# Performance work log

Hardware: AMD Instinct MI355X
Metric: run time of the kernel (lower is better)

## Reference

```python
import jax, jax.numpy as jnp
import numpy as np

N = 100000        # nodes
E = 3200000       # edges (avg degree 32)
B = 64            # graphs in the batch
IN_DIM = 128
HEADS = 4
C1 = 8            # conv1 out_channels per head
C2 = 4            # conv2 out_channels per head
OUT_DIM = 10
EPS = 1e-16       # PyG softmax denominator eps


def _lin(key, fan_in, fan_out):
    return jax.random.normal(key, (fan_in, fan_out), jnp.float32) / np.sqrt(fan_in)


def setup_inputs() -> dict:
    key = jax.random.key(0)
    ks = jax.random.split(key, 16)
    x = jax.random.normal(ks[0], (N, IN_DIM), jnp.float32)
    edge_index = jax.random.randint(ks[1], (2, E), 0, N)
    batch = jnp.sort(jax.random.randint(ks[2], (N,), 0, B))
    d1 = HEADS * C1  # 32
    d2 = HEADS * C2  # 16
    inp = {
        "x": x, "edge_index": edge_index, "batch": batch,
        # conv1 (TransformerConv in=128 -> heads*8 = 32)
        "Wq1": _lin(ks[3], IN_DIM, d1), "bq1": jnp.zeros((d1,), jnp.float32),
        "Wk1": _lin(ks[4], IN_DIM, d1), "bk1": jnp.zeros((d1,), jnp.float32),
        "Wv1": _lin(ks[5], IN_DIM, d1), "bv1": jnp.zeros((d1,), jnp.float32),
        "Ws1": _lin(ks[6], IN_DIM, d1), "bs1": jnp.zeros((d1,), jnp.float32),
        # conv2 (in=32 -> heads*4 = 16)
        "Wq2": _lin(ks[7], d1, d2), "bq2": jnp.zeros((d2,), jnp.float32),
        "Wk2": _lin(ks[8], d1, d2), "bk2": jnp.zeros((d2,), jnp.float32),
        "Wv2": _lin(ks[9], d1, d2), "bv2": jnp.zeros((d2,), jnp.float32),
        "Ws2": _lin(ks[10], d1, d2), "bs2": jnp.zeros((d2,), jnp.float32),
        # fc (16 -> 10)
        "Wfc": _lin(ks[11], d2, OUT_DIM), "bfc": jnp.zeros((OUT_DIM,), jnp.float32),
    }
    return inp


def transformer_conv(x, src, dst, Wq, bq, Wk, bk, Wv, bv, Ws, bs, heads):
    n = x.shape[0]
    hc = Wq.shape[1]
    c = hc // heads
    q = (x @ Wq + bq).reshape(n, heads, c)
    k = (x @ Wk + bk).reshape(n, heads, c)
    v = (x @ Wv + bv).reshape(n, heads, c)
    # edge-wise attention logits: query at dst, key at src -> [E, H]
    alpha = jnp.einsum('ehc,ehc->eh', q[dst], k[src]) / np.sqrt(c).astype(np.float32)
    # segment softmax over incoming edges of each dst node
    amax = jax.ops.segment_max(alpha, dst, num_segments=n)           # [N,H]
    ea = jnp.exp(alpha - amax[dst])
    denom = jax.ops.segment_sum(ea, dst, num_segments=n)             # [N,H]
    w = ea / (denom[dst] + EPS)                                      # [E,H]
    msg = v[src] * w[:, :, None]                                     # [E,H,C]
    out = jax.ops.segment_sum(msg, dst, num_segments=n).reshape(n, hc)
    return out + x @ Ws + bs  # root/skip connection


def reference(x, edge_index, batch,
              Wq1, bq1, Wk1, bk1, Wv1, bv1, Ws1, bs1,
              Wq2, bq2, Wk2, bk2, Wv2, bv2, Ws2, bs2,
              Wfc, bfc):
    src, dst = edge_index[0], edge_index[1]
    h = transformer_conv(x, src, dst, Wq1, bq1, Wk1, bk1, Wv1, bv1, Ws1, bs1, HEADS)
    h = jax.nn.relu(h)
    h = transformer_conv(h, src, dst, Wq2, bq2, Wk2, bk2, Wv2, bv2, Ws2, bs2, HEADS)
    h = jax.nn.relu(h)
    # global mean pool per graph
    sums = jax.ops.segment_sum(h, batch, num_segments=B)             # [B,16]
    cnt = jax.ops.segment_sum(jnp.ones((h.shape[0],), h.dtype), batch, num_segments=B)
    pooled = sums / jnp.maximum(cnt, 1.0)[:, None]
    return pooled @ Wfc + bfc                                        # [B,OUT_DIM]
```

## Files before the change

kernel.cpp:

```cpp
#include <hip/hip_runtime.h>

#define HEADS 4
#define EPS 1e-16f
#define NR 256
#define EPB 2048
#define XPAD 132

typedef float floatx2 __attribute__((ext_vector_type(2)));

__device__ inline int rangeOf(int dst, int rdiv, float rinv) {
    int q = (int)((float)dst * rinv);
    if (q > NR - 1) q = NR - 1;
    if ((long long)q * rdiv > dst) --q;
    else if ((long long)(q + 1) * rdiv <= dst) ++q;
    return q;
}

__global__ __launch_bounds__(256) void scatter_count(
    const int* __restrict__ ei, int E, int rdiv, float rinv,
    int* __restrict__ pcnt)
{
    __shared__ int cnt[NR];
    int b = blockIdx.x, t = threadIdx.x;
    int b0 = b * EPB;
    int nloc = min(EPB, E - b0);
    cnt[t] = 0;
    __syncthreads();
    #pragma unroll
    for (int u = 0; u < 8; ++u) {
        int li = u * 256 + t;
        if (li < nloc)
            atomicAdd(&cnt[rangeOf(ei[E + b0 + li], rdiv, rinv)], 1);
    }
    __syncthreads();
    pcnt[(size_t)b * NR + t] = cnt[t];
}

__global__ __launch_bounds__(256) void qprefix(
    int* __restrict__ pcnt, int nb, int* __restrict__ qtot)
{
    __shared__ int part[256];
    int q = blockIdx.x, t = threadIdx.x;
    int per = (nb + 255) >> 8;
    int lo = t * per, hi = min(lo + per, nb);
    int s = 0;
    for (int b = lo; b < hi; ++b) s += pcnt[(size_t)b * NR + q];
    part[t] = s;
    __syncthreads();
    for (int off = 1; off < 256; off <<= 1) {
        int a = (t >= off) ? part[t - off] : 0;
        __syncthreads();
        part[t] += a;
        __syncthreads();
    }
    if (t == 255) qtot[q] = part[255];
    int pre = (t == 0) ? 0 : part[t - 1];
    for (int b = lo; b < hi; ++b) {
        int c = pcnt[(size_t)b * NR + q];
        pcnt[(size_t)b * NR + q] = pre;
        pre += c;
    }
}

__global__ void qscan(const int* __restrict__ qtot, int* __restrict__ rstart)
{
    __shared__ int tmp[NR];
    int t = threadIdx.x;
    tmp[t] = qtot[t];
    __syncthreads();
    for (int off = 1; off < NR; off <<= 1) {
        int a = (t >= off) ? tmp[t - off] : 0;
        __syncthreads();
        tmp[t] += a;
        __syncthreads();
    }
    rstart[t] = (t == 0) ? 0 : tmp[t - 1];
    if (t == NR - 1) rstart[NR] = tmp[NR - 1];
}

__global__ __launch_bounds__(256) void scatter_place(
    const int* __restrict__ ei, int E, int rdiv, float rinv,
    const int* __restrict__ pcnt, const int* __restrict__ rstart,
    int* __restrict__ rsrc, int* __restrict__ rdst)
{
    __shared__ int2 lrec[EPB];
    __shared__ unsigned char lq[EPB];
    __shared__ int cnt[NR], base[NR], scn[NR];
    int b = blockIdx.x, t = threadIdx.x;
    int b0 = b * EPB;
    int nloc = min(EPB, E - b0);
    cnt[t] = 0;
    __syncthreads();
    int myq[8], myoff[8];
    int2 myrec[8];
    #pragma unroll
    for (int u = 0; u < 8; ++u) {
        int li = u * 256 + t;
        if (li < nloc) {
            int e = b0 + li;
            int sv = ei[e], dv = ei[E + e];
            int q = rangeOf(dv, rdiv, rinv);
            myq[u] = q;
            myrec[u] = make_int2(sv, dv);
            myoff[u] = atomicAdd(&cnt[q], 1);
        } else myq[u] = -1;
    }
    __syncthreads();
    scn[t] = cnt[t];
    __syncthreads();
    for (int off = 1; off < 256; off <<= 1) {
        int a = (t >= off) ? scn[t - off] : 0;
        __syncthreads();
        scn[t] += a;
        __syncthreads();
    }
    base[t] = (t == 0) ? 0 : scn[t - 1];
    __syncthreads();
    #pragma unroll
    for (int u = 0; u < 8; ++u) {
        if (myq[u] >= 0) {
            int slot = base[myq[u]] + myoff[u];
            lrec[slot] = myrec[u];
            lq[slot] = (unsigned char)myq[u];
        }
    }
    __syncthreads();
    #pragma unroll
    for (int u = 0; u < 8; ++u) {
        int s2 = u * 256 + t;
        if (s2 < nloc) {
            int q = lq[s2];
            int g = rstart[q] + pcnt[(size_t)b * NR + q] + (s2 - base[q]);
            int2 r = lrec[s2];
            rsrc[g] = r.x;
            rdst[g] = r.y;
        }
    }
}

__global__ __launch_bounds__(256) void deg_range(
    const int* __restrict__ rdst, const int* __restrict__ rstart,
    int* __restrict__ deg, int* __restrict__ row_ptr,
    int* __restrict__ phd, int n, int rdiv, int E)
{
    __shared__ int h[512];
    __shared__ int psum[256];
    __shared__ int hd[256];
    int q = blockIdx.x, t = threadIdx.x;
    int lo = q * rdiv, hi = min(lo + rdiv, n);
    int nn = hi - lo;
    if (nn <= 0) {
        phd[q * 256 + t] = 0;
        if (t == 0 && q == NR - 1) row_ptr[n] = E;
        return;
    }
    h[t] = 0; h[t + 256] = 0; hd[t] = 0;
    __syncthreads();
    int rlo = rstart[q], rhi = rstart[q + 1];
    for (int i = rlo + t; i < rhi; i += 256)
        atomicAdd(&h[rdst[i] - lo], 1);
    __syncthreads();
    int s0 = h[2 * t], s1 = h[2 * t + 1];
    psum[t] = s0 + s1;
    __syncthreads();
    for (int off = 1; off < 256; off <<= 1) {
        int a = (t >= off) ? psum[t - off] : 0;
        __syncthreads();
        psum[t] += a;
        __syncthreads();
    }
    int base = rlo + ((t == 0) ? 0 : psum[t - 1]);
    if (2 * t < nn) {
        row_ptr[lo + 2 * t] = base;
        deg[lo + 2 * t] = s0;
        atomicAdd(&hd[min(s0, 255)], 1);
    }
    if (2 * t + 1 < nn) {
        row_ptr[lo + 2 * t + 1] = base + s0;
        deg[lo + 2 * t + 1] = s1;
        atomicAdd(&hd[min(s1, 255)], 1);
    }
    if (t == 0 && q == NR - 1) row_ptr[n] = E;
    __syncthreads();
    phd[q * 256 + t] = hd[t];
}

__global__ __launch_bounds__(256) void dsort_scanA(
    int* __restrict__ phd, int* __restrict__ tot)
{
    __shared__ int tmp[256];
    int bin = blockIdx.x, t = threadIdx.x;
    int v = phd[t * 256 + bin];
    tmp[t] = v;
    __syncthreads();
    for (int off = 1; off < 256; off <<= 1) {
        int a = (t >= off) ? tmp[t - off] : 0;
        __syncthreads();
        tmp[t] += a;
        __syncthreads();
    }
    phd[t * 256 + bin] = tmp[t] - v;
    if (t == 255) tot[bin] = tmp[255];
}

__global__ void dsort_scanB(int* __restrict__ tot)
{
    __shared__ int tmp[256];
    int t = threadIdx.x;
    int v = tot[t];
    tmp[t] = v;
    __syncthreads();
    for (int off = 1; off < 256; off <<= 1) {
        int a = (t >= off) ? tmp[t - off] : 0;
        __syncthreads();
        tmp[t] += a;
        __syncthreads();
    }
    tot[t] = tmp[t] - v;
}

__global__ __launch_bounds__(256) void dsort_addC(
    int* __restrict__ phd, const int* __restrict__ tot)
{
    int t = threadIdx.x;
    phd[blockIdx.x * 256 + t] += tot[t];
}

__global__ __launch_bounds__(256) void place_range(
    const int* __restrict__ rsrc, const int* __restrict__ rdst,
    const int* __restrict__ rstart, const int* __restrict__ row_ptr,
    const int* __restrict__ deg, const int* __restrict__ phd,
    int* __restrict__ col, int* __restrict__ order, int n, int rdiv)
{
    __shared__ int cur[512];
    __shared__ int lcur[256];
    int q = blockIdx.x, t = threadIdx.x;
    int lo = q * rdiv, hi = min(lo + rdiv, n);
    int nn = hi - lo;
    if (nn <= 0) return;
    for (int i = t; i < nn; i += 256) cur[i] = row_ptr[lo + i];
    lcur[t] = phd[q * 256 + t];
    __syncthreads();
    int rlo = rstart[q], rhi = rstart[q + 1];
    for (int i = rlo + t; i < rhi; i += 256) {
        int pos = atomicAdd(&cur[rdst[i] - lo], 1);
        col[pos] = rsrc[i];
    }
    for (int i = t; i < nn; i += 256) {
        int pos = atomicAdd(&lcur[min(deg[lo + i], 255)], 1);
        order[pos] = lo + i;
    }
}

__global__ __launch_bounds__(256) void proj1_kernel(
    const float* __restrict__ x,
    const float* __restrict__ Wq, const float* __restrict__ bq,
    const float* __restrict__ Wk, const float* __restrict__ bk,
    const float* __restrict__ Wv, const float* __restrict__ bv,
    const float* __restrict__ Ws, const float* __restrict__ bs,
    float* __restrict__ qs1, unsigned char* __restrict__ kv1, int n)
{
    __shared__ float Wl[128][64];
    __shared__ float xl[64][XPAD];
    int half = blockIdx.x & 1;
    for (int i = threadIdx.x; i < 128 * 64; i += 256) {
        int k = i >> 6, c = i & 63;
        int gc = half * 64 + c;
        int sub = gc >> 5, j = gc & 31;
        const float* W = (sub == 0) ? Wq : (sub == 1) ? Wk : (sub == 2) ? Wv : Ws;
        Wl[k][c] = W[k * 32 + j];
    }
    int col4 = (threadIdx.x & 15) * 4;
    int gcol4 = half * 64 + col4;
    int sub = gcol4 >> 5, j = gcol4 & 31;
    float4 bias4;
    {
        const float* b = (sub == 0) ? bq : (sub == 1) ? bk : (sub == 2) ? bv : bs;
        bias4 = *(const float4*)(b + j);
    }
    int rb = (threadIdx.x >> 4) * 4;
    __syncthreads();
    int rstride = (gridDim.x >> 1) * 64;
    for (int row0 = (blockIdx.x >> 1) * 64; row0 < n; row0 += rstride) {
        #pragma unroll
        for (int u = 0; u < 8; ++u) {
            int i = threadIdx.x + u * 256;
            int r = i >> 5, c4 = (i & 31) * 4;
            int gr = row0 + r;
            float4 xv = (gr < n) ? *(const float4*)(x + (size_t)gr * 128 + c4)
                                 : make_float4(0.f, 0.f, 0.f, 0.f);
            *(float4*)(&xl[r][c4]) = xv;
        }
        __syncthreads();
        float4 a0 = bias4, a1 = bias4, a2 = bias4, a3 = bias4;
        #pragma unroll 2
        for (int k = 0; k < 128; k += 4) {
            float4 xv0 = *(const float4*)(&xl[rb + 0][k]);
            float4 xv1 = *(const float4*)(&xl[rb + 1][k]);
            float4 xv2 = *(const float4*)(&xl[rb + 2][k]);
            float4 xv3 = *(const float4*)(&xl[rb + 3][k]);
            float4 w0 = *(const float4*)(&Wl[k + 0][col4]);
            float4 w1 = *(const float4*)(&Wl[k + 1][col4]);
            float4 w2 = *(const float4*)(&Wl[k + 2][col4]);
            float4 w3 = *(const float4*)(&Wl[k + 3][col4]);
            a0.x += xv0.x*w0.x + xv0.y*w1.x + xv0.z*w2.x + xv0.w*w3.x;
            a0.y += xv0.x*w0.y + xv0.y*w1.y + xv0.z*w2.y + xv0.w*w3.y;
            a0.z += xv0.x*w0.z + xv0.y*w1.z + xv0.z*w2.z + xv0.w*w3.z;
            a0.w += xv0.x*w0.w + xv0.y*w1.w + xv0.z*w2.w + xv0.w*w3.w;
            a1.x += xv1.x*w0.x + xv1.y*w1.x + xv1.z*w2.x + xv1.w*w3.x;
            a1.y += xv1.x*w0.y + xv1.y*w1.y + xv1.z*w2.y + xv1.w*w3.y;
            a1.z += xv1.x*w0.z + xv1.y*w1.z + xv1.z*w2.z + xv1.w*w3.z;
            a1.w += xv1.x*w0.w + xv1.y*w1.w + xv1.z*w2.w + xv1.w*w3.w;
            a2.x += xv2.x*w0.x + xv2.y*w1.x + xv2.z*w2.x + xv2.w*w3.x;
            a2.y += xv2.x*w0.y + xv2.y*w1.y + xv2.z*w2.y + xv2.w*w3.y;
            a2.z += xv2.x*w0.z + xv2.y*w1.z + xv2.z*w2.z + xv2.w*w3.z;
            a2.w += xv2.x*w0.w + xv2.y*w1.w + xv2.z*w2.w + xv2.w*w3.w;
            a3.x += xv3.x*w0.x + xv3.y*w1.x + xv3.z*w2.x + xv3.w*w3.x;
            a3.y += xv3.x*w0.y + xv3.y*w1.y + xv3.z*w2.y + xv3.w*w3.y;
            a3.z += xv3.x*w0.z + xv3.y*w1.z + xv3.z*w2.z + xv3.w*w3.z;
            a3.w += xv3.x*w0.w + xv3.y*w1.w + xv3.z*w2.w + xv3.w*w3.w;
        }
        #pragma unroll
        for (int r = 0; r < 4; ++r) {
            int row = row0 + rb + r;
            if (row < n) {
                float4 acc = (r == 0) ? a0 : (r == 1) ? a1 : (r == 2) ? a2 : a3;
                if (sub == 0)
                    *(float4*)(qs1 + (size_t)row * 64 + j) = acc;
                else if (sub == 3)
                    *(float4*)(qs1 + (size_t)row * 64 + 32 + j) = acc;
                else {
                    unsigned u8 = __builtin_amdgcn_cvt_pk_fp8_f32(acc.x, acc.y, 0u, false);
                    u8 = __builtin_amdgcn_cvt_pk_fp8_f32(acc.z, acc.w, u8, true);
                    *(unsigned*)(kv1 + (size_t)row * 64 + ((sub == 1) ? 0 : 32) + j) = u8;
                }
            }
        }
        __syncthreads();
    }
}

__global__ __launch_bounds__(256) void proj2_kernel(
    const float* __restrict__ h1,
    const float* __restrict__ Wq, const float* __restrict__ bq,
    const float* __restrict__ Wk, const float* __restrict__ bk,
    const float* __restrict__ Wv, const float* __restrict__ bv,
    const float* __restrict__ Ws, const float* __restrict__ bs,
    float* __restrict__ qs2, unsigned char* __restrict__ kv2, int n)
{
    __shared__ float Wl[32][64];
    __shared__ float bl[64];
    __shared__ float xl[4][32];
    for (int i = threadIdx.x; i < 32 * 64; i += 256) {
        int k = i >> 6, c = i & 63;
        int sub = c >> 4, j = c & 15;
        const float* W = (sub == 0) ? Wq : (sub == 1) ? Wk : (sub == 2) ? Wv : Ws;
        Wl[k][c] = W[k * 16 + j];
    }
    if (threadIdx.x < 64) {
        int c = threadIdx.x, sub = c >> 4, j = c & 15;
        const float* b = (sub == 0) ? bq : (sub == 1) ? bk : (sub == 2) ? bv : bs;
        bl[c] = b[j];
    }
    __syncthreads();
    int r = threadIdx.x >> 6, col = threadIdx.x & 63;
    int sub = col >> 4, j = col & 15;
    for (int row0 = blockIdx.x * 4; row0 < n; row0 += gridDim.x * 4) {
        int li = threadIdx.x;
        if (li < 128) {
            int rr = row0 + (li >> 5);
            if (rr < n) xl[li >> 5][li & 31] = h1[(size_t)rr * 32 + (li & 31)];
        }
        __syncthreads();
        int row = row0 + r;
        if (row < n) {
            float acc = bl[col];
            #pragma unroll
            for (int k = 0; k < 32; ++k) acc += xl[r][k] * Wl[k][col];
            if (sub == 0)       qs2[(size_t)row * 32 + j] = acc;
            else if (sub == 3)  qs2[(size_t)row * 32 + 16 + j] = acc;
            else {
                unsigned u8 = __builtin_amdgcn_cvt_pk_fp8_f32(acc, 0.f, 0u, false);
                kv2[(size_t)row * 32 + ((sub == 1) ? 0 : 16) + j] = (unsigned char)(u8 & 0xFF);
            }
        }
        __syncthreads();
    }
}

__global__ __launch_bounds__(256) void gather_conv1(
    const int* __restrict__ row_ptr, const int* __restrict__ order,
    const int* __restrict__ col, const float* __restrict__ qs1,
    const unsigned char* __restrict__ kv1, float* __restrict__ h1, int n)
{
    int tid = blockIdx.x * 256 + threadIdx.x;
    if (tid >= n * HEADS) return;
    int node = order[tid >> 2], h = tid & 3;
    const float4* qp = (const float4*)(qs1 + (size_t)node * 64 + h * 8);
    float4 q0 = qp[0], q1 = qp[1];
    int start = row_ptr[node], d = row_ptr[node + 1] - start;
    float m = -INFINITY, s = 0.f;
    float a0x=0,a0y=0,a0z=0,a0w=0,a1x=0,a1y=0,a1z=0,a1w=0;
    uint2 ku = make_uint2(0,0), vu = make_uint2(0,0);
    if (d > 0) {
        const unsigned char* b0 = kv1 + (size_t)col[start] * 64;
        ku = *(const uint2*)(b0 + h * 8);
        vu = *(const uint2*)(b0 + 32 + h * 8);
    }
    for (int i = 0; i < d; ++i) {
        uint2 kn = ku, vn = vu;
        if (i + 1 < d) {
            const unsigned char* nb = kv1 + (size_t)col[start + i + 1] * 64;
            kn = *(const uint2*)(nb + h * 8);
            vn = *(const uint2*)(nb + 32 + h * 8);
        }
        floatx2 k01 = __builtin_amdgcn_cvt_pk_f32_fp8(ku.x, false);
        floatx2 k23 = __builtin_amdgcn_cvt_pk_f32_fp8(ku.x, true);
        floatx2 k45 = __builtin_amdgcn_cvt_pk_f32_fp8(ku.y, false);
        floatx2 k67 = __builtin_amdgcn_cvt_pk_f32_fp8(ku.y, true);
        float a = (q0.x*k01.x + q0.y*k01.y + q0.z*k23.x + q0.w*k23.y
                 + q1.x*k45.x + q1.y*k45.y + q1.z*k67.x + q1.w*k67.y)
                * 0.35355339059327373f;
        float mn = fmaxf(m, a);
        float corr = __expf(m - mn);
        float ea = __expf(a - mn);
        s = s * corr + ea;
        floatx2 v01 = __builtin_amdgcn_cvt_pk_f32_fp8(vu.x, false);
        floatx2 v23 = __builtin_amdgcn_cvt_pk_f32_fp8(vu.x, true);
        floatx2 v45 = __builtin_amdgcn_cvt_pk_f32_fp8(vu.y, false);
        floatx2 v67 = __builtin_amdgcn_cvt_pk_f32_fp8(vu.y, true);
        a0x = a0x*corr + ea*v01.x; a0y = a0y*corr + ea*v01.y;
        a0z = a0z*corr + ea*v23.x; a0w = a0w*corr + ea*v23.y;
        a1x = a1x*corr + ea*v45.x; a1y = a1y*corr + ea*v45.y;
        a1z = a1z*corr + ea*v67.x; a1w = a1w*corr + ea*v67.y;
        m = mn;
        ku = kn; vu = vn;
    }
    float inv = 1.f / (s + EPS);
    const float* sk = qs1 + (size_t)node * 64 + 32 + h * 8;
    float4 o0, o1;
    o0.x = fmaxf(a0x*inv + sk[0], 0.f); o0.y = fmaxf(a0y*inv + sk[1], 0.f);
    o0.z = fmaxf(a0z*inv + sk[2], 0.f); o0.w = fmaxf(a0w*inv + sk[3], 0.f);
    o1.x = fmaxf(a1x*inv + sk[4], 0.f); o1.y = fmaxf(a1y*inv + sk[5], 0.f);
    o1.z = fmaxf(a1z*inv + sk[6], 0.f); o1.w = fmaxf(a1w*inv + sk[7], 0.f);
    float4* op = (float4*)(h1 + (size_t)node * 32 + h * 8);
    op[0] = o0; op[1] = o1;
}

__global__ __launch_bounds__(256) void gather_conv2(
    const int* __restrict__ row_ptr, const int* __restrict__ order,
    const int* __restrict__ col, const float* __restrict__ qs2,
    const unsigned char* __restrict__ kv2, float* __restrict__ h2, int n)
{
    int tid = blockIdx.x * 256 + threadIdx.x;
    if (tid >= n * HEADS) return;
    int node = order[tid >> 2], h = tid & 3;
    float4 q = *(const float4*)(qs2 + (size_t)node * 32 + h * 4);
    int start = row_ptr[node], d = row_ptr[node + 1] - start;
    float m = -INFINITY, s = 0.f;
    float ax=0, ay=0, az=0, aw=0;
    unsigned ku = 0, vu = 0;
    if (d > 0) {
        const unsigned char* b0 = kv2 + (size_t)col[start] * 32;
        ku = *(const unsigned*)(b0 + h * 4);
        vu = *(const unsigned*)(b0 + 16 + h * 4);
    }
    for (int i = 0; i < d; ++i) {
        unsigned kn = ku, vn = vu;
        if (i + 1 < d) {
            const unsigned char* nb = kv2 + (size_t)col[start + i + 1] * 32;
            kn = *(const unsigned*)(nb + h * 4);
            vn = *(const unsigned*)(nb + 16 + h * 4);
        }
        floatx2 k01 = __builtin_amdgcn_cvt_pk_f32_fp8(ku, false);
        floatx2 k23 = __builtin_amdgcn_cvt_pk_f32_fp8(ku, true);
        float a = (q.x*k01.x + q.y*k01.y + q.z*k23.x + q.w*k23.y) * 0.5f;
        float mn = fmaxf(m, a);
        float corr = __expf(m - mn);
        float ea = __expf(a - mn);
        s = s * corr + ea;
        floatx2 v01 = __builtin_amdgcn_cvt_pk_f32_fp8(vu, false);
        floatx2 v23 = __builtin_amdgcn_cvt_pk_f32_fp8(vu, true);
        ax = ax*corr + ea*v01.x; ay = ay*corr + ea*v01.y;
        az = az*corr + ea*v23.x; aw = aw*corr + ea*v23.y;
        m = mn;
        ku = kn; vu = vn;
    }
    float inv = 1.f / (s + EPS);
    const float* sk = qs2 + (size_t)node * 32 + 16 + h * 4;
    float4 o;
    o.x = fmaxf(ax*inv + sk[0], 0.f);
    o.y = fmaxf(ay*inv + sk[1], 0.f);
    o.z = fmaxf(az*inv + sk[2], 0.f);
    o.w = fmaxf(aw*inv + sk[3], 0.f);
    *(float4*)(h2 + (size_t)node * 16 + h * 4) = o;
}

__global__ __launch_bounds__(256) void pool_kernel(
    const float* __restrict__ h2, const int* __restrict__ batch,
    float* __restrict__ pooled, float* __restrict__ cnt, int n)
{
    __shared__ float acc[16];
    __shared__ int bShared;
    __shared__ int uniform;
    int node0 = blockIdx.x * 16;
    int t = threadIdx.x;
    int node = node0 + (t >> 4), j = t & 15;
    if (t == 0) {
        int bFirst = batch[node0];
        int bLast = batch[min(node0 + 15, n - 1)];
        bShared = bFirst;
        uniform = (bFirst == bLast);
    }
    if (t < 16) acc[t] = 0.f;
    __syncthreads();
    bool active = node < n;
    float val = active ? h2[(size_t)node * 16 + j] : 0.f;
    if (uniform) {
        if (active) atomicAdd(&acc[j], val);
        __syncthreads();
        int nlocal = min(16, n - node0);
        if (t < 16) atomicAdd(pooled + bShared * 16 + t, acc[t]);
        if (t == 0) atomicAdd(cnt + bShared, (float)nlocal);
    } else {
        if (active) {
            int b = batch[node];
            atomicAdd(pooled + b * 16 + j, val);
            if (j == 0) atomicAdd(cnt + b, 1.f);
        }
    }
}

__global__ void fc_kernel(
    const float* __restrict__ pooled, const float* __restrict__ cnt,
    const float* __restrict__ Wfc, const float* __restrict__ bfc,
    float* __restrict__ out)
{
    int t = threadIdx.x;
    if (t < 64 * 10) {
        int b = t / 10, o = t % 10;
        float c = fmaxf(cnt[b], 1.0f);
        float acc = bfc[o];
        #pragma unroll
        for (int k = 0; k < 16; ++k)
            acc += (pooled[b * 16 + k] / c) * Wfc[k * 10 + o];
        out[t] = acc;
    }
}

extern "C" void kernel_launch(void* const* d_in, const int* in_sizes, int n_in,
                              void* d_out, int out_size, void* d_ws, size_t ws_size,
                              hipStream_t stream) {
    const float* x     = (const float*)d_in[0];
    const int*   ei    = (const int*)d_in[1];
    const int*   batch = (const int*)d_in[2];
    const float* Wq1 = (const float*)d_in[3],  *bq1 = (const float*)d_in[4];
    const float* Wk1 = (const float*)d_in[5],  *bk1 = (const float*)d_in[6];
    const float* Wv1 = (const float*)d_in[7],  *bv1 = (const float*)d_in[8];
    const float* Ws1 = (const float*)d_in[9],  *bs1 = (const float*)d_in[10];
    const float* Wq2 = (const float*)d_in[11], *bq2 = (const float*)d_in[12];
    const float* Wk2 = (const float*)d_in[13], *bk2 = (const float*)d_in[14];
    const float* Wv2 = (const float*)d_in[15], *bv2 = (const float*)d_in[16];
    const float* Ws2 = (const float*)d_in[17], *bs2 = (const float*)d_in[18];
    const float* Wfc = (const float*)d_in[19], *bfc = (const float*)d_in[20];

    int N = in_sizes[0] / 128;
    int E = in_sizes[1] / 2;
    int rdiv = (N + NR - 1) / NR;
    float rinv = 1.0f / (float)rdiv;
    int NB = (E + EPB - 1) / EPB;

    float* ws = (float*)d_ws;
    float* qs1    = ws;
    float* h1     = qs1 + (size_t)N * 64;
    float* h2     = h1 + (size_t)N * 32;
    float* qs2    = h2 + (size_t)N * 16;
    float* pooled = qs2 + (size_t)N * 32;
    float* cnt    = pooled + 1024;
    unsigned char* kv1 = (unsigned char*)(cnt + 64);
    unsigned char* kv2 = kv1 + (size_t)N * 64;
    int* deg     = (int*)(kv2 + (size_t)N * 32);
    int* row_ptr = deg + N;
    int* rstart  = row_ptr + N + 1;
    int* qtot    = rstart + NR + 1;
    int* col     = qtot + NR;
    int* order   = col + E;
    int* pcnt    = order + N;
    int* phd     = pcnt + (size_t)NB * NR;
    int* rsrc = (int*)h1;
    int* rdst = (int*)h2;

    hipMemsetAsync(pooled, 0, (1024 + 64) * sizeof(float), stream);

    int ngrid = (N * HEADS + 255) / 256;

    scatter_count<<<NB, 256, 0, stream>>>(ei, E, rdiv, rinv, pcnt);
    qprefix<<<NR, 256, 0, stream>>>(pcnt, NB, qtot);
    qscan<<<1, NR, 0, stream>>>(qtot, rstart);
    scatter_place<<<NB, 256, 0, stream>>>(ei, E, rdiv, rinv, pcnt, rstart, rsrc, rdst);
    deg_range<<<NR, 256, 0, stream>>>(rdst, rstart, deg, row_ptr, phd, N, rdiv, E);
    dsort_scanA<<<NR, 256, 0, stream>>>(phd, qtot);
    dsort_scanB<<<1, 256, 0, stream>>>(qtot);
    dsort_addC<<<NR, 256, 0, stream>>>(phd, qtot);
    place_range<<<NR, 256, 0, stream>>>(rsrc, rdst, rstart, row_ptr, deg, phd, col, order, N, rdiv);

    proj1_kernel<<<2048, 256, 0, stream>>>(x, Wq1, bq1, Wk1, bk1, Wv1, bv1, Ws1, bs1, qs1, kv1, N);
    gather_conv1<<<ngrid, 256, 0, stream>>>(row_ptr, order, col, qs1, kv1, h1, N);

    proj2_kernel<<<1024, 256, 0, stream>>>(h1, Wq2, bq2, Wk2, bk2, Wv2, bv2, Ws2, bs2, qs2, kv2, N);
    gather_conv2<<<ngrid, 256, 0, stream>>>(row_ptr, order, col, qs2, kv2, h2, N);

    pool_kernel<<<(N + 15) / 16, 256, 0, stream>>>(h2, batch, pooled, cnt, N);
    fc_kernel<<<1, 640, 0, stream>>>(pooled, cnt, Wfc, bfc, (float*)d_out);
}
```

Before: 372.6 us.

## Restructure projection kernels to one row per thread with register accumulators

Both projection kernels now assign one node row per thread with 64 register accumulators, staging x in 16-column shared-memory chunks. The weights are read directly from global memory as uniform, broadcast-friendly loads instead of being staged in LDS. Each thread writes its full output row with vectorized stores, including packed fp8 K/V. The aim is to cut LDS traffic and weight-staging overhead and to make proj2's stores wider. The cost is high register pressure (64 accumulators), which may reduce occupancy, and more global weight loads.

```diff
diff --git a/kernel.cpp b/kernel.cpp
--- a/kernel.cpp
+++ b/kernel.cpp
@@ -4,7 +4,6 @@
 #define EPS 1e-16f
 #define NR 256
 #define EPB 2048
-#define XPAD 132
 
 typedef float floatx2 __attribute__((ext_vector_type(2)));
 
@@ -260,83 +259,73 @@
     const float* __restrict__ Ws, const float* __restrict__ bs,
     float* __restrict__ qs1, unsigned char* __restrict__ kv1, int n)
 {
-    __shared__ float Wl[128][64];
-    __shared__ float xl[64][XPAD];
+    __shared__ float xl[256][20];
     int half = blockIdx.x & 1;
-    for (int i = threadIdx.x; i < 128 * 64; i += 256) {
-        int k = i >> 6, c = i & 63;
-        int gc = half * 64 + c;
-        int sub = gc >> 5, j = gc & 31;
-        const float* W = (sub == 0) ? Wq : (sub == 1) ? Wk : (sub == 2) ? Wv : Ws;
-        Wl[k][c] = W[k * 32 + j];
-    }
-    int col4 = (threadIdx.x & 15) * 4;
-    int gcol4 = half * 64 + col4;
-    int sub = gcol4 >> 5, j = gcol4 & 31;
-    float4 bias4;
-    {
-        const float* b = (sub == 0) ? bq : (sub == 1) ? bk : (sub == 2) ? bv : bs;
-        bias4 = *(const float4*)(b + j);
-    }
-    int rb = (threadIdx.x >> 4) * 4;
-    __syncthreads();
-    int rstride = (gridDim.x >> 1) * 64;
-    for (int row0 = (blockIdx.x >> 1) * 64; row0 < n; row0 += rstride) {
+    const float* WA = half ? Wv : Wq;
+    const float* WB = half ? Ws : Wk;
+    const float* bA = half ? bv : bq;
+    const float* bB = half ? bs : bk;
+    int row0 = (blockIdx.x >> 1) * 256;
+    int t = threadIdx.x;
+    int row = row0 + t;
+    float acc[64];
+    #pragma unroll
+    for (int c = 0; c < 32; ++c) { acc[c] = bA[c]; acc[32 + c] = bB[c]; }
+    for (int kc = 0; kc < 128; kc += 16) {
         #pragma unroll
-        for (int u = 0; u < 8; ++u) {
-            int i = threadIdx.x + u * 256;
-            int r = i >> 5, c4 = (i & 31) * 4;
+        for (int u = 0; u < 4; ++u) {
+            int i = t + u * 256;
+            int r = i >> 2, f = i & 3;
             int gr = row0 + r;
-            float4 xv = (gr < n) ? *(const float4*)(x + (size_t)gr * 128 + c4)
+            float4 xv = (gr < n) ? *(const float4*)(x + (size_t)gr * 128 + kc + f * 4)
                                  : make_float4(0.f, 0.f, 0.f, 0.f);
-            *(float4*)(&xl[r][c4]) = xv;
-        }
-        __syncthreads();
-        float4 a0 = bias4, a1 = bias4, a2 = bias4, a3 = bias4;
+            *(float4*)(&xl[r][f * 4]) = xv;
+        }
+        __syncthreads();
         #pragma unroll 2
-        for (int k = 0; k < 128; k += 4) {
-            float4 xv0 = *(const float4*)(&xl[rb + 0][k]);
-            float4 xv1 = *(const float4*)(&xl[rb + 1][k]);
-            float4 xv2 = *(const float4*)(&xl[rb + 2][k]);
-            float4 xv3 = *(const float4*)(&xl[rb + 3][k]);
-            float4 w0 = *(const float4*)(&Wl[k + 0][col4]);
-            float4 w1 = *(const float4*)(&Wl[k + 1][col4]);
-            float4 w2 = *(const float4*)(&Wl[k + 2][col4]);
-            float4 w3 = *(const float4*)(&Wl[k + 3][col4]);
-            a0.x += xv0.x*w0.x + xv0.y*w1.x + xv0.z*w2.x + xv0.w*w3.x;
-            a0.y += xv0.x*w0.y + xv0.y*w1.y + xv0.z*w2.y + xv0.w*w3.y;
-            a0.z += xv0.x*w0.z + xv0.y*w1.z + xv0.z*w2.z + xv0.w*w3.z;
-            a0.w += xv0.x*w0.w + xv0.y*w1.w + xv0.z*w2.w + xv0.w*w3.w;
-            a1.x += xv1.x*w0.x + xv1.y*w1.x + xv1.z*w2.x + xv1.w*w3.x;
-            a1.y += xv1.x*w0.y + xv1.y*w1.y + xv1.z*w2.y + xv1.w*w3.y;
-            a1.z += xv1.x*w0.z + xv1.y*w1.z + xv1.z*w2.z + xv1.w*w3.z;
-            a1.w += xv1.x*w0.w + xv1.y*w1.w + xv1.z*w2.w + xv1.w*w3.w;
-            a2.x += xv2.x*w0.x + xv2.y*w1.x + xv2.z*w2.x + xv2.w*w3.x;
-            a2.y += xv2.x*w0.y + xv2.y*w1.y + xv2.z*w2.y + xv2.w*w3.y;
-            a2.z += xv2.x*w0.z + xv2.y*w1.z + xv2.z*w2.z + xv2.w*w3.z;
-            a2.w += xv2.x*w0.w + xv2.y*w1.w + xv2.z*w2.w + xv2.w*w3.w;
-            a3.x += xv3.x*w0.x + xv3.y*w1.x + xv3.z*w2.x + xv3.w*w3.x;
-            a3.y += xv3.x*w0.y + xv3.y*w1.y + xv3.z*w2.y + xv3.w*w3.y;
-            a3.z += xv3.x*w0.z + xv3.y*w1.z + xv3.z*w2.z + xv3.w*w3.z;
-            a3.w += xv3.x*w0.w + xv3.y*w1.w + xv3.z*w2.w + xv3.w*w3.w;
-        }
-        #pragma unroll
-        for (int r = 0; r < 4; ++r) {
-            int row = row0 + rb + r;
-            if (row < n) {
-                float4 acc = (r == 0) ? a0 : (r == 1) ? a1 : (r == 2) ? a2 : a3;
-                if (sub == 0)
-                    *(float4*)(qs1 + (size_t)row * 64 + j) = acc;
-                else if (sub == 3)
-                    *(float4*)(qs1 + (size_t)row * 64 + 32 + j) = acc;
-                else {
-                    unsigned u8 = __builtin_amdgcn_cvt_pk_fp8_f32(acc.x, acc.y, 0u, false);
-                    u8 = __builtin_amdgcn_cvt_pk_fp8_f32(acc.z, acc.w, u8, true);
-                    *(unsigned*)(kv1 + (size_t)row * 64 + ((sub == 1) ? 0 : 32) + j) = u8;
-                }
+        for (int kk = 0; kk < 16; ++kk) {
+            int k = kc + kk;
+            float xs = xl[t][kk];
+            const float* wa = WA + k * 32;
+            const float* wb = WB + k * 32;
+            #pragma unroll
+            for (int c = 0; c < 32; ++c) {
+                acc[c]      += xs * wa[c];
+                acc[32 + c] += xs * wb[c];
             }
         }
         __syncthreads();
+    }
+    if (row < n) {
+        if (half == 0) {
+            #pragma unroll
+            for (int cg = 0; cg < 8; ++cg)
+                *(float4*)(qs1 + (size_t)row * 64 + cg * 4) =
+                    make_float4(acc[cg*4], acc[cg*4+1], acc[cg*4+2], acc[cg*4+3]);
+            unsigned w[8];
+            #pragma unroll
+            for (int g = 0; g < 8; ++g) {
+                unsigned u8 = __builtin_amdgcn_cvt_pk_fp8_f32(acc[32+g*4], acc[32+g*4+1], 0u, false);
+                u8 = __builtin_amdgcn_cvt_pk_fp8_f32(acc[32+g*4+2], acc[32+g*4+3], u8, true);
+                w[g] = u8;
+            }
+            *(uint4*)(kv1 + (size_t)row * 64)      = make_uint4(w[0], w[1], w[2], w[3]);
+            *(uint4*)(kv1 + (size_t)row * 64 + 16) = make_uint4(w[4], w[5], w[6], w[7]);
+        } else {
+            unsigned w[8];
+            #pragma unroll
+            for (int g = 0; g < 8; ++g) {
+                unsigned u8 = __builtin_amdgcn_cvt_pk_fp8_f32(acc[g*4], acc[g*4+1], 0u, false);
+                u8 = __builtin_amdgcn_cvt_pk_fp8_f32(acc[g*4+2], acc[g*4+3], u8, true);
+                w[g] = u8;
+            }
+            *(uint4*)(kv1 + (size_t)row * 64 + 32) = make_uint4(w[0], w[1], w[2], w[3]);
+            *(uint4*)(kv1 + (size_t)row * 64 + 48) = make_uint4(w[4], w[5], w[6], w[7]);
+            #pragma unroll
+            for (int cg = 0; cg < 8; ++cg)
+                *(float4*)(qs1 + (size_t)row * 64 + 32 + cg * 4) =
+                    make_float4(acc[32+cg*4], acc[32+cg*4+1], acc[32+cg*4+2], acc[32+cg*4+3]);
+        }
     }
 }
 
@@ -348,43 +337,66 @@
     const float* __restrict__ Ws, const float* __restrict__ bs,
     float* __restrict__ qs2, unsigned char* __restrict__ kv2, int n)
 {
-    __shared__ float Wl[32][64];
-    __shared__ float bl[64];
-    __shared__ float xl[4][32];
-    for (int i = threadIdx.x; i < 32 * 64; i += 256) {
-        int k = i >> 6, c = i & 63;
-        int sub = c >> 4, j = c & 15;
-        const float* W = (sub == 0) ? Wq : (sub == 1) ? Wk : (sub == 2) ? Wv : Ws;
-        Wl[k][c] = W[k * 16 + j];
-    }
-    if (threadIdx.x < 64) {
-        int c = threadIdx.x, sub = c >> 4, j = c & 15;
-        const float* b = (sub == 0) ? bq : (sub == 1) ? bk : (sub == 2) ? bv : bs;
-        bl[c] = b[j];
-    }
-    __syncthreads();
-    int r = threadIdx.x >> 6, col = threadIdx.x & 63;
-    int sub = col >> 4, j = col & 15;
-    for (int row0 = blockIdx.x * 4; row0 < n; row0 += gridDim.x * 4) {
-        int li = threadIdx.x;
-        if (li < 128) {
-            int rr = row0 + (li >> 5);
-            if (rr < n) xl[li >> 5][li & 31] = h1[(size_t)rr * 32 + (li & 31)];
-        }
-        __syncthreads();
-        int row = row0 + r;
-        if (row < n) {
-            float acc = bl[col];
+    __shared__ float xl[256][20];
+    int row0 = blockIdx.x * 256;
+    int t = threadIdx.x;
+    int row = row0 + t;
+    float acc[64];
+    #pragma unroll
+    for (int c = 0; c < 16; ++c) {
+        acc[c] = bq[c]; acc[16 + c] = bk[c];
+        acc[32 + c] = bv[c]; acc[48 + c] = bs[c];
+    }
+    for (int kc = 0; kc < 32; kc += 16) {
+        #pragma unroll
+        for (int u = 0; u < 4; ++u) {
+            int i = t + u * 256;
+            int r = i >> 2, f = i & 3;
+            int gr = row0 + r;
+            float4 xv = (gr < n) ? *(const float4*)(h1 + (size_t)gr * 32 + kc + f * 4)
+                                 : make_float4(0.f, 0.f, 0.f, 0.f);
+            *(float4*)(&xl[r][f * 4]) = xv;
+        }
+        __syncthreads();
+        #pragma unroll 2
+        for (int kk = 0; kk < 16; ++kk) {
+            int k = kc + kk;
+            float xs = xl[t][kk];
+            const float* w0 = Wq + k * 16;
+            const float* w1 = Wk + k * 16;
+            const float* w2 = Wv + k * 16;
+            const float* w3 = Ws + k * 16;
             #pragma unroll
-            for (int k = 0; k < 32; ++k) acc += xl[r][k] * Wl[k][col];
-            if (sub == 0)       qs2[(size_t)row * 32 + j] = acc;
-            else if (sub == 3)  qs2[(size_t)row * 32 + 16 + j] = acc;
-            else {
-                unsigned u8 = __builtin_amdgcn_cvt_pk_fp8_f32(acc, 0.f, 0u, false);
-                kv2[(size_t)row * 32 + ((sub == 1) ? 0 : 16) + j] = (unsigned char)(u8 & 0xFF);
+            for (int c = 0; c < 16; ++c) {
+                acc[c]      += xs * w0[c];
+                acc[16 + c] += xs * w1[c];
+                acc[32 + c] += xs * w2[c];
+                acc[48 + c] += xs * w3[c];
             }
         }
         __syncthreads();
+    }
+    if (row < n) {
+        #pragma unroll
+        for (int cg = 0; cg < 4; ++cg)
+            *(float4*)(qs2 + (size_t)row * 32 + cg * 4) =
+                make_float4(acc[cg*4], acc[cg*4+1], acc[cg*4+2], acc[cg*4+3]);
+        #pragma unroll
+        for (int cg = 0; cg < 4; ++cg)
+            *(float4*)(qs2 + (size_t)row * 32 + 16 + cg * 4) =
+                make_float4(acc[48+cg*4], acc[48+cg*4+1], acc[48+cg*4+2], acc[48+cg*4+3]);
+        unsigned wk_[4], wv_[4];
+        #pragma unroll
+        for (int g = 0; g < 4; ++g) {
+            unsigned u8 = __builtin_amdgcn_cvt_pk_fp8_f32(acc[16+g*4], acc[16+g*4+1], 0u, false);
+            u8 = __builtin_amdgcn_cvt_pk_fp8_f32(acc[16+g*4+2], acc[16+g*4+3], u8, true);
+            wk_[g] = u8;
+            unsigned v8 = __builtin_amdgcn_cvt_pk_fp8_f32(acc[32+g*4], acc[32+g*4+1], 0u, false);
+            v8 = __builtin_amdgcn_cvt_pk_fp8_f32(acc[32+g*4+2], acc[32+g*4+3], v8, true);
+            wv_[g] = v8;
+        }
+        *(uint4*)(kv2 + (size_t)row * 32)      = make_uint4(wk_[0], wk_[1], wk_[2], wk_[3]);
+        *(uint4*)(kv2 + (size_t)row * 32 + 16) = make_uint4(wv_[0], wv_[1], wv_[2], wv_[3]);
     }
 }
 
@@ -593,6 +605,7 @@
     hipMemsetAsync(pooled, 0, (1024 + 64) * sizeof(float), stream);
 
     int ngrid = (N * HEADS + 255) / 256;
+    int ptiles = (N + 255) / 256;
 
     scatter_count<<<NB, 256, 0, stream>>>(ei, E, rdiv, rinv, pcnt);
     qprefix<<<NR, 256, 0, stream>>>(pcnt, NB, qtot);
@@ -604,10 +617,10 @@
     dsort_addC<<<NR, 256, 0, stream>>>(phd, qtot);
     place_range<<<NR, 256, 0, stream>>>(rsrc, rdst, rstart, row_ptr, deg, phd, col, order, N, rdiv);
 
-    proj1_kernel<<<2048, 256, 0, stream>>>(x, Wq1, bq1, Wk1, bk1, Wv1, bv1, Ws1, bs1, qs1, kv1, N);
+    proj1_kernel<<<2 * ptiles, 256, 0, stream>>>(x, Wq1, bq1, Wk1, bk1, Wv1, bv1, Ws1, bs1, qs1, kv1, N);
     gather_conv1<<<ngrid, 256, 0, stream>>>(row_ptr, order, col, qs1, kv1, h1, N);
 
-    proj2_kernel<<<1024, 256, 0, stream>>>(h1, Wq2, bq2, Wk2, bk2, Wv2, bv2, Ws2, bs2, qs2, kv2, N);
+    proj2_kernel<<<ptiles, 256, 0, stream>>>(h1, Wq2, bq2, Wk2, bk2, Wv2, bv2, Ws2, bs2, qs2, kv2, N);
     gather_conv2<<<ngrid, 256, 0, stream>>>(row_ptr, order, col, qs2, kv2, h2, N);
 
     pool_kernel<<<(N + 15) / 16, 256, 0, stream>>>(h2, batch, pooled, cnt, N);
```

New measurement: 376.7 us. About the same (+1.1%).

## Use bf16 MFMA for both projection GEMMs with prepacked weights

Applied to the files above, without the earlier changes.

Both node projection kernels are rewritten to use 16x16x32 bf16 MFMA instructions in place of FP32 FMA loops over LDS tiles. Weights are packed once per call into the MFMA B-operand layout by two small kernels, and activations are converted to bf16 in registers. This removes the LDS staging and scalar FMA cost of the projections. In exchange, inputs and weights are rounded to bf16, which adds error, the output stores become scalar and strided, and two extra launches are added.

```diff
diff --git a/kernel.cpp b/kernel.cpp
--- a/kernel.cpp
+++ b/kernel.cpp
@@ -4,9 +4,19 @@
 #define EPS 1e-16f
 #define NR 256
 #define EPB 2048
-#define XPAD 132
 
 typedef float floatx2 __attribute__((ext_vector_type(2)));
+typedef short bf16x8 __attribute__((ext_vector_type(8)));
+typedef float f32x4 __attribute__((ext_vector_type(4)));
+
+__device__ inline unsigned short f2bf(float f) {
+    union { float f; unsigned u; } v; v.f = f;
+    unsigned r = v.u + 0x7FFFu + ((v.u >> 16) & 1u);
+    return (unsigned short)(r >> 16);
+}
+__device__ inline unsigned char f2fp8(float f) {
+    return (unsigned char)(__builtin_amdgcn_cvt_pk_fp8_f32(f, 0.f, 0u, false) & 0xFF);
+}
 
 __device__ inline int rangeOf(int dst, int rdiv, float rinv) {
     int q = (int)((float)dst * rinv);
@@ -252,139 +262,155 @@
     }
 }
 
-__global__ __launch_bounds__(256) void proj1_kernel(
-    const float* __restrict__ x,
-    const float* __restrict__ Wq, const float* __restrict__ bq,
-    const float* __restrict__ Wk, const float* __restrict__ bk,
-    const float* __restrict__ Wv, const float* __restrict__ bv,
-    const float* __restrict__ Ws, const float* __restrict__ bs,
+__global__ __launch_bounds__(256) void pack_w1(
+    const float* __restrict__ Wq, const float* __restrict__ Wk,
+    const float* __restrict__ Wv, const float* __restrict__ Ws,
+    unsigned short* __restrict__ wp)
+{
+    int tid = blockIdx.x * 256 + threadIdx.x;
+    int s = tid >> 9, c = (tid >> 6) & 7, l = tid & 63;
+    int gcol = c * 16 + (l & 15);
+    int sub = gcol >> 5, j = gcol & 31;
+    const float* W = (sub == 0) ? Wq : (sub == 1) ? Wk : (sub == 2) ? Wv : Ws;
+    int k0 = s * 32 + ((l >> 4) << 3);
+    unsigned short v[8];
+    #pragma unroll
+    for (int jj = 0; jj < 8; ++jj) v[jj] = f2bf(W[(size_t)(k0 + jj) * 32 + j]);
+    uint4 o;
+    o.x = v[0] | ((unsigned)v[1] << 16);
+    o.y = v[2] | ((unsigned)v[3] << 16);
+    o.z = v[4] | ((unsigned)v[5] << 16);
+    o.w = v[6] | ((unsigned)v[7] << 16);
+    *(uint4*)(wp + (size_t)tid * 8) = o;
+}
+
+__global__ void pack_w2(
+    const float* __restrict__ Wq, const float* __restrict__ Wk,
+    const float* __restrict__ Wv, const float* __restrict__ Ws,
+    unsigned short* __restrict__ wp)
+{
+    int tid = threadIdx.x;
+    int c = tid >> 6, l = tid & 63;
+    int gcol = c * 16 + (l & 15);
+    int sub = gcol >> 4, j = gcol & 15;
+    const float* W = (sub == 0) ? Wq : (sub == 1) ? Wk : (sub == 2) ? Wv : Ws;
+    int k0 = (l >> 4) << 3;
+    unsigned short v[8];
+    #pragma unroll
+    for (int jj = 0; jj < 8; ++jj) v[jj] = f2bf(W[(size_t)(k0 + jj) * 16 + j]);
+    uint4 o;
+    o.x = v[0] | ((unsigned)v[1] << 16);
+    o.y = v[2] | ((unsigned)v[3] << 16);
+    o.z = v[4] | ((unsigned)v[5] << 16);
+    o.w = v[6] | ((unsigned)v[7] << 16);
+    *(uint4*)(wp + (size_t)tid * 8) = o;
+}
+
+__global__ __launch_bounds__(256) void proj1_mfma(
+    const float* __restrict__ x, const unsigned short* __restrict__ wp,
+    const float* __restrict__ bq, const float* __restrict__ bk,
+    const float* __restrict__ bv, const float* __restrict__ bs,
     float* __restrict__ qs1, unsigned char* __restrict__ kv1, int n)
 {
-    __shared__ float Wl[128][64];
-    __shared__ float xl[64][XPAD];
-    int half = blockIdx.x & 1;
-    for (int i = threadIdx.x; i < 128 * 64; i += 256) {
-        int k = i >> 6, c = i & 63;
-        int gc = half * 64 + c;
-        int sub = gc >> 5, j = gc & 31;
-        const float* W = (sub == 0) ? Wq : (sub == 1) ? Wk : (sub == 2) ? Wv : Ws;
-        Wl[k][c] = W[k * 32 + j];
-    }
-    int col4 = (threadIdx.x & 15) * 4;
-    int gcol4 = half * 64 + col4;
-    int sub = gcol4 >> 5, j = gcol4 & 31;
-    float4 bias4;
-    {
-        const float* b = (sub == 0) ? bq : (sub == 1) ? bk : (sub == 2) ? bv : bs;
-        bias4 = *(const float4*)(b + j);
-    }
-    int rb = (threadIdx.x >> 4) * 4;
-    __syncthreads();
-    int rstride = (gridDim.x >> 1) * 64;
-    for (int row0 = (blockIdx.x >> 1) * 64; row0 < n; row0 += rstride) {
-        #pragma unroll
-        for (int u = 0; u < 8; ++u) {
-            int i = threadIdx.x + u * 256;
-            int r = i >> 5, c4 = (i & 31) * 4;
-            int gr = row0 + r;
-            float4 xv = (gr < n) ? *(const float4*)(x + (size_t)gr * 128 + c4)
-                                 : make_float4(0.f, 0.f, 0.f, 0.f);
-            *(float4*)(&xl[r][c4]) = xv;
-        }
-        __syncthreads();
-        float4 a0 = bias4, a1 = bias4, a2 = bias4, a3 = bias4;
-        #pragma unroll 2
-        for (int k = 0; k < 128; k += 4) {
-            float4 xv0 = *(const float4*)(&xl[rb + 0][k]);
-            float4 xv1 = *(const float4*)(&xl[rb + 1][k]);
-            float4 xv2 = *(const float4*)(&xl[rb + 2][k]);
-            float4 xv3 = *(const float4*)(&xl[rb + 3][k]);
-            float4 w0 = *(const float4*)(&Wl[k + 0][col4]);
-            float4 w1 = *(const float4*)(&Wl[k + 1][col4]);
-            float4 w2 = *(const float4*)(&Wl[k + 2][col4]);
-            float4 w3 = *(const float4*)(&Wl[k + 3][col4]);
-            a0.x += xv0.x*w0.x + xv0.y*w1.x + xv0.z*w2.x + xv0.w*w3.x;
-            a0.y += xv0.x*w0.y + xv0.y*w1.y + xv0.z*w2.y + xv0.w*w3.y;
-            a0.z += xv0.x*w0.z + xv0.y*w1.z + xv0.z*w2.z + xv0.w*w3.z;
-            a0.w += xv0.x*w0.w + xv0.y*w1.w + xv0.z*w2.w + xv0.w*w3.w;
-            a1.x += xv1.x*w0.x + xv1.y*w1.x + xv1.z*w2.x + xv1.w*w3.x;
-            a1.y += xv1.x*w0.y + xv1.y*w1.y + xv1.z*w2.y + xv1.w*w3.y;
-            a1.z += xv1.x*w0.z + xv1.y*w1.z + xv1.z*w2.z + xv1.w*w3.z;
-            a1.w += xv1.x*w0.w + xv1.y*w1.w + xv1.z*w2.w + xv1.w*w3.w;
-            a2.x += xv2.x*w0.x + xv2.y*w1.x + xv2.z*w2.x + xv2.w*w3.x;
-            a2.y += xv2.x*w0.y + xv2.y*w1.y + xv2.z*w2.y + xv2.w*w3.y;
-            a2.z += xv2.x*w0.z + xv2.y*w1.z + xv2.z*w2.z + xv2.w*w3.z;
-            a2.w += xv2.x*w0.w + xv2.y*w1.w + xv2.z*w2.w + xv2.w*w3.w;
-            a3.x += xv3.x*w0.x + xv3.y*w1.x + xv3.z*w2.x + xv3.w*w3.x;
-            a3.y += xv3.x*w0.y + xv3.y*w1.y + xv3.z*w2.y + xv3.w*w3.y;
-            a3.z += xv3.x*w0.z + xv3.y*w1.z + xv3.z*w2.z + xv3.w*w3.z;
-            a3.w += xv3.x*w0.w + xv3.y*w1.w + xv3.z*w2.w + xv3.w*w3.w;
-        }
-        #pragma unroll
-        for (int r = 0; r < 4; ++r) {
-            int row = row0 + rb + r;
-            if (row < n) {
-                float4 acc = (r == 0) ? a0 : (r == 1) ? a1 : (r == 2) ? a2 : a3;
-                if (sub == 0)
-                    *(float4*)(qs1 + (size_t)row * 64 + j) = acc;
-                else if (sub == 3)
-                    *(float4*)(qs1 + (size_t)row * 64 + 32 + j) = acc;
-                else {
-                    unsigned u8 = __builtin_amdgcn_cvt_pk_fp8_f32(acc.x, acc.y, 0u, false);
-                    u8 = __builtin_amdgcn_cvt_pk_fp8_f32(acc.z, acc.w, u8, true);
-                    *(unsigned*)(kv1 + (size_t)row * 64 + ((sub == 1) ? 0 : 32) + j) = u8;
-                }
-            }
-        }
-        __syncthreads();
-    }
-}
-
-__global__ __launch_bounds__(256) void proj2_kernel(
-    const float* __restrict__ h1,
-    const float* __restrict__ Wq, const float* __restrict__ bq,
-    const float* __restrict__ Wk, const float* __restrict__ bk,
-    const float* __restrict__ Wv, const float* __restrict__ bv,
-    const float* __restrict__ Ws, const float* __restrict__ bs,
+    int w = threadIdx.x >> 6, l = threadIdx.x & 63;
+    int row0 = blockIdx.x * 64 + w * 16;
+    if (row0 >= n) return;
+    int arow = row0 + (l & 15);
+    f32x4 c0 = {0,0,0,0}, c1 = {0,0,0,0}, c2 = {0,0,0,0}, c3 = {0,0,0,0};
+    f32x4 c4 = {0,0,0,0}, c5 = {0,0,0,0}, c6 = {0,0,0,0}, c7 = {0,0,0,0};
+    const uint4* wp4 = (const uint4*)wp;
+    #pragma unroll
+    for (int s = 0; s < 4; ++s) {
+        union { uint4 u; bf16x8 b; } av;
+        if (arow < n) {
+            const float* xp = x + (size_t)arow * 128 + s * 32 + ((l >> 4) << 3);
+            float4 x0 = *(const float4*)xp;
+            float4 x1 = *(const float4*)(xp + 4);
+            av.u.x = f2bf(x0.x) | ((unsigned)f2bf(x0.y) << 16);
+            av.u.y = f2bf(x0.z) | ((unsigned)f2bf(x0.w) << 16);
+            av.u.z = f2bf(x1.x) | ((unsigned)f2bf(x1.y) << 16);
+            av.u.w = f2bf(x1.z) | ((unsigned)f2bf(x1.w) << 16);
+        } else {
+            av.u = make_uint4(0, 0, 0, 0);
+        }
+        const uint4* base = wp4 + (size_t)(s * 8) * 64 + l;
+        union { uint4 u; bf16x8 b; } bc;
+        bc.u = base[0 * 64]; c0 = __builtin_amdgcn_mfma_f32_16x16x32_bf16(av.b, bc.b, c0, 0, 0, 0);
+        bc.u = base[1 * 64]; c1 = __builtin_amdgcn_mfma_f32_16x16x32_bf16(av.b, bc.b, c1, 0, 0, 0);
+        bc.u = base[2 * 64]; c2 = __builtin_amdgcn_mfma_f32_16x16x32_bf16(av.b, bc.b, c2, 0, 0, 0);
+        bc.u = base[3 * 64]; c3 = __builtin_amdgcn_mfma_f32_16x16x32_bf16(av.b, bc.b, c3, 0, 0, 0);
+        bc.u = base[4 * 64]; c4 = __builtin_amdgcn_mfma_f32_16x16x32_bf16(av.b, bc.b, c4, 0, 0, 0);
+        bc.u = base[5 * 64]; c5 = __builtin_amdgcn_mfma_f32_16x16x32_bf16(av.b, bc.b, c5, 0, 0, 0);
+        bc.u = base[6 * 64]; c6 = __builtin_amdgcn_mfma_f32_16x16x32_bf16(av.b, bc.b, c6, 0, 0, 0);
+        bc.u = base[7 * 64]; c7 = __builtin_amdgcn_mfma_f32_16x16x32_bf16(av.b, bc.b, c7, 0, 0, 0);
+    }
+    int rbase = row0 + ((l >> 4) << 2);
+    int lc = l & 15;
+    float bq0 = bq[lc], bq1 = bq[16 + lc];
+    float bk0 = bk[lc], bk1 = bk[16 + lc];
+    float bv0 = bv[lc], bv1 = bv[16 + lc];
+    float bs0 = bs[lc], bs1 = bs[16 + lc];
+    #pragma unroll
+    for (int r = 0; r < 4; ++r) {
+        int row = rbase + r;
+        if (row < n) {
+            float* q = qs1 + (size_t)row * 64;
+            unsigned char* kvp = kv1 + (size_t)row * 64;
+            q[lc]      = c0[r] + bq0;
+            q[16 + lc] = c1[r] + bq1;
+            q[32 + lc] = c6[r] + bs0;
+            q[48 + lc] = c7[r] + bs1;
+            kvp[lc]      = f2fp8(c2[r] + bk0);
+            kvp[16 + lc] = f2fp8(c3[r] + bk1);
+            kvp[32 + lc] = f2fp8(c4[r] + bv0);
+            kvp[48 + lc] = f2fp8(c5[r] + bv1);
+        }
+    }
+}
+
+__global__ __launch_bounds__(256) void proj2_mfma(
+    const float* __restrict__ h1, const unsigned short* __restrict__ wp,
+    const float* __restrict__ bq, const float* __restrict__ bk,
+    const float* __restrict__ bv, const float* __restrict__ bs,
     float* __restrict__ qs2, unsigned char* __restrict__ kv2, int n)
 {
-    __shared__ float Wl[32][64];
-    __shared__ float bl[64];
-    __shared__ float xl[4][32];
-    for (int i = threadIdx.x; i < 32 * 64; i += 256) {
-        int k = i >> 6, c = i & 63;
-        int sub = c >> 4, j = c & 15;
-        const float* W = (sub == 0) ? Wq : (sub == 1) ? Wk : (sub == 2) ? Wv : Ws;
-        Wl[k][c] = W[k * 16 + j];
-    }
-    if (threadIdx.x < 64) {
-        int c = threadIdx.x, sub = c >> 4, j = c & 15;
-        const float* b = (sub == 0) ? bq : (sub == 1) ? bk : (sub == 2) ? bv : bs;
-        bl[c] = b[j];
-    }
-    __syncthreads();
-    int r = threadIdx.x >> 6, col = threadIdx.x & 63;
-    int sub = col >> 4, j = col & 15;
-    for (int row0 = blockIdx.x * 4; row0 < n; row0 += gridDim.x * 4) {
-        int li = threadIdx.x;
-        if (li < 128) {
-            int rr = row0 + (li >> 5);
-            if (rr < n) xl[li >> 5][li & 31] = h1[(size_t)rr * 32 + (li & 31)];
-        }
-        __syncthreads();
-        int row = row0 + r;
+    int w = threadIdx.x >> 6, l = threadIdx.x & 63;
+    int row0 = blockIdx.x * 64 + w * 16;
+    if (row0 >= n) return;
+    int arow = row0 + (l & 15);
+    f32x4 c0 = {0,0,0,0}, c1 = {0,0,0,0}, c2 = {0,0,0,0}, c3 = {0,0,0,0};
+    union { uint4 u; bf16x8 b; } av;
+    if (arow < n) {
+        const float* xp = h1 + (size_t)arow * 32 + ((l >> 4) << 3);
+        float4 x0 = *(const float4*)xp;
+        float4 x1 = *(const float4*)(xp + 4);
+        av.u.x = f2bf(x0.x) | ((unsigned)f2bf(x0.y) << 16);
+        av.u.y = f2bf(x0.z) | ((unsigned)f2bf(x0.w) << 16);
+        av.u.z = f2bf(x1.x) | ((unsigned)f2bf(x1.y) << 16);
+        av.u.w = f2bf(x1.z) | ((unsigned)f2bf(x1.w) << 16);
+    } else {
+        av.u = make_uint4(0, 0, 0, 0);
+    }
+    const uint4* base = (const uint4*)wp + l;
+    union { uint4 u; bf16x8 b; } bc;
+    bc.u = base[0];   c0 = __builtin_amdgcn_mfma_f32_16x16x32_bf16(av.b, bc.b, c0, 0, 0, 0);
+    bc.u = base[64];  c1 = __builtin_amdgcn_mfma_f32_16x16x32_bf16(av.b, bc.b, c1, 0, 0, 0);
+    bc.u = base[128]; c2 = __builtin_amdgcn_mfma_f32_16x16x32_bf16(av.b, bc.b, c2, 0, 0, 0);
+    bc.u = base[192]; c3 = __builtin_amdgcn_mfma_f32_16x16x32_bf16(av.b, bc.b, c3, 0, 0, 0);
+    int rbase = row0 + ((l >> 4) << 2);
+    int lc = l & 15;
+    float bq0 = bq[lc], bk0 = bk[lc], bv0 = bv[lc], bs0 = bs[lc];
+    #pragma unroll
+    for (int r = 0; r < 4; ++r) {
+        int row = rbase + r;
         if (row < n) {
-            float acc = bl[col];
-            #pragma unroll
-            for (int k = 0; k < 32; ++k) acc += xl[r][k] * Wl[k][col];
-            if (sub == 0)       qs2[(size_t)row * 32 + j] = acc;
-            else if (sub == 3)  qs2[(size_t)row * 32 + 16 + j] = acc;
-            else {
-                unsigned u8 = __builtin_amdgcn_cvt_pk_fp8_f32(acc, 0.f, 0u, false);
-                kv2[(size_t)row * 32 + ((sub == 1) ? 0 : 16) + j] = (unsigned char)(u8 & 0xFF);
-            }
-        }
-        __syncthreads();
+            float* q = qs2 + (size_t)row * 32;
+            unsigned char* kvp = kv2 + (size_t)row * 32;
+            q[lc]        = c0[r] + bq0;
+            q[16 + lc]   = c3[r] + bs0;
+            kvp[lc]      = f2fp8(c1[r] + bk0);
+            kvp[16 + lc] = f2fp8(c2[r] + bv0);
+        }
     }
 }
 
@@ -587,12 +613,18 @@
     int* order   = col + E;
     int* pcnt    = order + N;
     int* phd     = pcnt + (size_t)NB * NR;
+    unsigned short* wp1 = (unsigned short*)(phd + (size_t)NR * 256);
+    unsigned short* wp2 = wp1 + 16384;
     int* rsrc = (int*)h1;
     int* rdst = (int*)h2;
 
     hipMemsetAsync(pooled, 0, (1024 + 64) * sizeof(float), stream);
 
     int ngrid = (N * HEADS + 255) / 256;
+    int mtiles = (N + 63) / 64;
+
+    pack_w1<<<8, 256, 0, stream>>>(Wq1, Wk1, Wv1, Ws1, wp1);
+    pack_w2<<<1, 256, 0, stream>>>(Wq2, Wk2, Wv2, Ws2, wp2);
 
     scatter_count<<<NB, 256, 0, stream>>>(ei, E, rdiv, rinv, pcnt);
     qprefix<<<NR, 256, 0, stream>>>(pcnt, NB, qtot);
@@ -604,10 +636,10 @@
     dsort_addC<<<NR, 256, 0, stream>>>(phd, qtot);
     place_range<<<NR, 256, 0, stream>>>(rsrc, rdst, rstart, row_ptr, deg, phd, col, order, N, rdiv);
 
-    proj1_kernel<<<2048, 256, 0, stream>>>(x, Wq1, bq1, Wk1, bk1, Wv1, bv1, Ws1, bs1, qs1, kv1, N);
+    proj1_mfma<<<mtiles, 256, 0, stream>>>(x, wp1, bq1, bk1, bv1, bs1, qs1, kv1, N);
     gather_conv1<<<ngrid, 256, 0, stream>>>(row_ptr, order, col, qs1, kv1, h1, N);
 
-    proj2_kernel<<<1024, 256, 0, stream>>>(h1, Wq2, bq2, Wk2, bk2, Wv2, bv2, Ws2, bs2, qs2, kv2, N);
+    proj2_mfma<<<mtiles, 256, 0, stream>>>(h1, wp2, bq2, bk2, bv2, bs2, qs2, kv2, N);
     gather_conv2<<<ngrid, 256, 0, stream>>>(row_ptr, order, col, qs2, kv2, h2, N);
 
     pool_kernel<<<(N + 15) / 16, 256, 0, stream>>>(h2, batch, pooled, cnt, N);
```

Result: faster. 318.7 us (-14.5%).
